# Kernel optimization log

Hardware: AMD Instinct MI355X
Metric: run time of the kernel (lower is better)

Reference implementation:

```python
import jax, jax.numpy as jnp
import numpy as np

B, S, D, H, P, K = 2, 1025, 1024, 16, 1024, 32
HD = D // H
G = int(np.sqrt(P))
TEMP = 0.1
CANTOR_W = 0.3
SCALE = HD ** -0.5
EPS_LN = 1e-5


def _layernorm(x, w, b):
    m = jnp.mean(x, axis=-1, keepdims=True)
    v = jnp.mean((x - m) ** 2, axis=-1, keepdims=True)
    return (x - m) * jax.lax.rsqrt(v + EPS_LN) * w + b


def _l2norm(x):
    n = jnp.sqrt(jnp.sum(x * x, axis=-1, keepdims=True))
    return x / jnp.maximum(n, 1e-12)


def _cantor_bias():
    idx = np.arange(P)
    xg, yg = idx % G, idx // G
    s = xg + yg
    z = (s * (s + 1) // 2 + yg).astype(np.float32)
    fp = z / max(z.max(), 1.0)
    dist = np.abs(fp[None, :] - fp[:, None])
    aff = 1.0 - dist
    np.fill_diagonal(aff, -1e9)
    return jnp.asarray(aff * CANTOR_W, dtype=jnp.float32)


def setup_inputs() -> dict:
    key = jax.random.key(0)
    ks = jax.random.split(key, 16)
    std = 0.02
    def w(k, *shape):
        return jax.random.normal(k, shape, dtype=jnp.float32) * std
    inp = {
        'x': jax.random.normal(ks[0], (B, S, D), dtype=jnp.float32),
        'norm1_w': jnp.ones((D,), jnp.float32), 'norm1_b': jnp.zeros((D,), jnp.float32),
        'rq_w': w(ks[1], D, D), 'rq_b': jnp.zeros((D,), jnp.float32),
        'rk_w': w(ks[2], D, D), 'rk_b': jnp.zeros((D,), jnp.float32),
        'pos_bias': _cantor_bias(),
        'qkv_w': w(ks[3], 3 * D, D), 'qkv_b': jnp.zeros((3 * D,), jnp.float32),
        'proj_w': w(ks[4], D, D), 'proj_b': jnp.zeros((D,), jnp.float32),
        'norm2_w': jnp.ones((D,), jnp.float32), 'norm2_b': jnp.zeros((D,), jnp.float32),
        'fc1_w': w(ks[5], 4 * D, D), 'fc1_b': jnp.zeros((4 * D,), jnp.float32),
        'fc2_w': w(ks[6], D, 4 * D), 'fc2_b': jnp.zeros((D,), jnp.float32),
    }
    return inp


def reference(x, norm1_w, norm1_b, rq_w, rq_b, rk_w, rk_b, pos_bias,
              qkv_w, qkv_b, proj_w, proj_b, norm2_w, norm2_b,
              fc1_w, fc1_b, fc2_w, fc2_b):
    x_norm = _layernorm(x, norm1_w, norm1_b)
    # ---- router: content-based top-k wormhole routes over patches ----
    xp = x_norm[:, 1:, :]                                   # [B,P,D]
    q_r = _l2norm(xp @ rq_w.T + rq_b)
    k_r = _l2norm(xp @ rk_w.T + rk_b)
    scores = jnp.einsum('bpd,bqd->bpq', q_r, k_r) + pos_bias[None]
    eye = jnp.eye(P, dtype=bool)
    scores = jnp.where(eye[None], -1e9, scores)
    topk_scores, routes = jax.lax.top_k(scores / TEMP, K)   # [B,P,K]
    route_w = jax.nn.softmax(topk_scores, axis=-1)          # [B,P,K]
    # ---- qkv ----
    qkv = (x_norm @ qkv_w.T + qkv_b).reshape(B, S, 3, H, HD)
    qkv = jnp.transpose(qkv, (2, 0, 3, 1, 4))               # [3,B,H,S,hd]
    Q, Kf, V = qkv[0], qkv[1], qkv[2]
    # CLS token: dense attention over all positions
    Qc = Q[:, :, :1, :]
    attn_cls = jax.nn.softmax(jnp.einsum('bhqd,bhkd->bhqk', Qc, Kf) * SCALE, axis=-1)
    out_cls = jnp.einsum('bhqk,bhkd->bhqd', attn_cls, V)    # [B,H,1,hd]
    # Patches: sparse gather attention via wormhole routes
    Qp, Kp, Vp = Q[:, :, 1:], Kf[:, :, 1:], V[:, :, 1:]     # [B,H,P,hd]
    gather = jax.vmap(lambda t, r: t[:, r])                 # t:[H,P,hd], r:[P,K] -> [H,P,K,hd]
    Kg = gather(Kp, routes)                                  # [B,H,P,K,hd]
    Vg = gather(Vp, routes)
    sp = jnp.einsum('bhpd,bhpkd->bhpk', Qp, Kg) * SCALE
    sp = sp + jnp.clip(jnp.log(route_w), -10.0, None)[:, None]
    attn_p = jax.nn.softmax(sp, axis=-1)
    out_p = jnp.einsum('bhpk,bhpkd->bhpd', attn_p, Vg)      # [B,H,P,hd]
    out = jnp.concatenate([out_cls, out_p], axis=2)          # [B,H,S,hd]
    out = jnp.transpose(out, (0, 2, 1, 3)).reshape(B, S, D)
    x = x + (out @ proj_w.T + proj_b)
    h = _layernorm(x, norm2_w, norm2_b)
    h = jax.nn.gelu(h @ fc1_w.T + fc1_b, approximate=False)
    x = x + (h @ fc2_w.T + fc2_b)
    return x
```

## Files before the change

### kernel.cpp

```cpp
#include <hip/hip_runtime.h>
#include <hip/hip_bf16.h>
#include <math.h>

typedef unsigned short u16;
typedef __attribute__((ext_vector_type(8))) short short8;
typedef __attribute__((ext_vector_type(4))) float f32x4;

#define B_ 2
#define S_ 1025
#define D_ 1024
#define H_ 16
#define HD_ 64
#define P_ 1024
#define K_ 32
#define NS_ 16

static constexpr float TEMP_ = 0.1f;
static constexpr float SCALE_ = 0.125f;
static constexpr float EPS_LN_ = 1e-5f;

__device__ __forceinline__ float bf2f(u16 u) {
  unsigned int t = ((unsigned int)u) << 16;
  float f;
  __builtin_memcpy(&f, &t, 4);
  return f;
}
__device__ __forceinline__ u16 f2bf(float f) {
  __hip_bfloat16 h = __float2bfloat16(f);
  u16 u;
  __builtin_memcpy(&u, &h, 2);
  return u;
}
__device__ __forceinline__ float gelu_f(float x) {
  return 0.5f * x * (1.0f + erff(x * 0.70710678118654752f));
}

typedef __attribute__((address_space(1))) const unsigned int gas_u32;
typedef __attribute__((address_space(3))) unsigned int las_u32;
__device__ __forceinline__ void g2l16(const void* g, void* l) {
  __builtin_amdgcn_global_load_lds((gas_u32*)g, (las_u32*)l, 16, 0, 0);
}

__global__ __launch_bounds__(256) void conv4_kernel(
    const float* __restrict__ s0, int n0, const float* __restrict__ s1, int n1,
    const float* __restrict__ s2, int n2, const float* __restrict__ s3, int n3,
    u16* __restrict__ dst) {
  const int e = (blockIdx.x * 256 + threadIdx.x) * 4;
  const float* src;
  int off;
  if (e < n0) { src = s0; off = e; }
  else if (e < n0 + n1) { src = s1; off = e - n0; }
  else if (e < n0 + n1 + n2) { src = s2; off = e - n0 - n1; }
  else if (e < n0 + n1 + n2 + n3) { src = s3; off = e - n0 - n1 - n2; }
  else return;
  float4 t = *reinterpret_cast<const float4*>(src + off);
  ushort4 o;
  o.x = f2bf(t.x); o.y = f2bf(t.y); o.z = f2bf(t.z); o.w = f2bf(t.w);
  *reinterpret_cast<ushort4*>(dst + e) = o;
}

__global__ __launch_bounds__(256) void init_addb(const float* __restrict__ a,
                                                 const float* __restrict__ bias,
                                                 float* __restrict__ out) {
  const long long base = (long long)blockIdx.x * D_;
#pragma unroll
  for (int u = 0; u < 4; ++u) {
    int d = threadIdx.x + u * 256;
    out[base + d] = a[base + d] + bias[d];
  }
}

__global__ __launch_bounds__(256) void init_scores(const float* __restrict__ pos,
                                                   float* __restrict__ scores) {
  const int bp = blockIdx.x;
  const int p = bp & (P_ - 1);
  const long long base = (long long)bp * P_;
#pragma unroll
  for (int u = 0; u < 4; ++u) {
    int q = threadIdx.x + u * 256;
    float v = pos[(long long)p * P_ + q];
    if (p == q) v = -1e9f;
    scores[base + q] = v;
  }
}

__device__ __forceinline__ float block_sum256(float v, float* red4) {
  for (int off = 32; off > 0; off >>= 1) v += __shfl_down(v, off);
  if ((threadIdx.x & 63) == 0) red4[threadIdx.x >> 6] = v;
  __syncthreads();
  float r = red4[0] + red4[1] + red4[2] + red4[3];
  __syncthreads();
  return r;
}
__device__ __forceinline__ float block_max256(float v, float* red4) {
  for (int off = 32; off > 0; off >>= 1) v = fmaxf(v, __shfl_down(v, off));
  if ((threadIdx.x & 63) == 0) red4[threadIdx.x >> 6] = v;
  __syncthreads();
  float r = fmaxf(fmaxf(red4[0], red4[1]), fmaxf(red4[2], red4[3]));
  __syncthreads();
  return r;
}

__global__ __launch_bounds__(256) void ln_kernel(const float* __restrict__ x,
                                                 const float* __restrict__ w,
                                                 const float* __restrict__ b,
                                                 u16* __restrict__ out) {
  __shared__ float red4[4];
  const long long base = (long long)blockIdx.x * D_;
  float v[4];
  float s = 0.f, ss = 0.f;
#pragma unroll
  for (int u = 0; u < 4; ++u) {
    int d = threadIdx.x + u * 256;
    float f = x[base + d];
    v[u] = f; s += f; ss += f * f;
  }
  float tot = block_sum256(s, red4);
  float tot2 = block_sum256(ss, red4);
  float mean = tot * (1.0f / D_);
  float var = tot2 * (1.0f / D_) - mean * mean;
  float rstd = rsqrtf(var + EPS_LN_);
#pragma unroll
  for (int u = 0; u < 4; ++u) {
    int d = threadIdx.x + u * 256;
    out[base + d] = f2bf((v[u] - mean) * rstd * w[d] + b[d]);
  }
}

__global__ __launch_bounds__(256) void l2norm2_kernel(u16* __restrict__ qr,
                                                      u16* __restrict__ kr) {
  __shared__ float red4[4];
  const int row = blockIdx.x;
  u16* x = (row < 2048) ? qr + (long long)row * D_
                        : kr + (long long)(row - 2048) * D_;
  float v[4];
  float ss = 0.f;
#pragma unroll
  for (int u = 0; u < 4; ++u) {
    int d = threadIdx.x + u * 256;
    v[u] = bf2f(x[d]);
    ss += v[u] * v[u];
  }
  float tot = block_sum256(ss, red4);
  float inv = 1.0f / fmaxf(sqrtf(tot), 1e-12f);
#pragma unroll
  for (int u = 0; u < 4; ++u) {
    int d = threadIdx.x + u * 256;
    x[d] = f2bf(v[u] * inv);
  }
}

template <int MODE>
__device__ __forceinline__ void gemm_body(
    u16* sA, u16* sW,
    const u16* __restrict__ A, long long a_off, const u16* __restrict__ W,
    int N, int M, int Kd, int klen, int rpb, long long a_bs, long long w_bs,
    const float* __restrict__ bias, const float* __restrict__ bias2, int bias_off,
    u16* __restrict__ outU, u16* __restrict__ outU2, float* __restrict__ outF,
    int bx, int by, int bz) {
  const int tid = threadIdx.x;
  const int lane = tid & 63;
  const int q4 = lane >> 4;
  const int r16 = lane & 15;
  const int wave = tid >> 6;
  const int wr = (wave >> 1) * 64;
  const int wc = (wave & 1) * 64;
  const int row0 = by * 128;
  const int col0 = bx * 128;
  const int batch = row0 / rpb;
  const u16* Ab = A + a_off + (long long)batch * a_bs +
                  (long long)(row0 - batch * rpb) * Kd;
  const u16* Wb = W + (long long)batch * w_bs + (long long)col0 * Kd;
  const int rmax = N - 1 - row0;
  const int srow = tid >> 3;
  const int kx = ((tid & 7) ^ (srow & 7)) * 8;
  const int kbeg = bz * klen;
  const int niter = klen >> 6;
  f32x4 acc[4][4] = {};
  for (int it = 0; it < niter; ++it) {
    const int k0 = kbeg + it * 64;
#pragma unroll
    for (int c = 0; c < 4; ++c) {
      const int rg = c * 32 + srow;
      g2l16(Ab + (long long)min(rg, rmax) * Kd + kx + k0, &sA[c * 2048 + tid * 8]);
      g2l16(Wb + (long long)rg * Kd + kx + k0, &sW[c * 2048 + tid * 8]);
    }
    __builtin_amdgcn_s_waitcnt(0);
    __syncthreads();
#pragma unroll
    for (int s = 0; s < 2; ++s) {
      short8 a[4], b[4];
      const int ks = ((s * 4 + q4) ^ (r16 & 7)) * 8;
#pragma unroll
      for (int i = 0; i < 4; ++i) {
        a[i] = *reinterpret_cast<const short8*>(&sA[(wr + i * 16 + r16) * 64 + ks]);
        b[i] = *reinterpret_cast<const short8*>(&sW[(wc + i * 16 + r16) * 64 + ks]);
      }
#pragma unroll
      for (int i = 0; i < 4; ++i)
#pragma unroll
        for (int j = 0; j < 4; ++j)
          acc[i][j] = __builtin_amdgcn_mfma_f32_16x16x32_bf16(a[i], b[j],
                                                              acc[i][j], 0, 0, 0);
    }
    __syncthreads();
  }
#pragma unroll
  for (int i = 0; i < 4; ++i) {
#pragma unroll
    for (int reg = 0; reg < 4; ++reg) {
      const int n = row0 + wr + i * 16 + q4 * 4 + reg;
      if (n >= N) continue;
      const long long nrow = (long long)n * M;
#pragma unroll
      for (int j = 0; j < 4; ++j) {
        const int m = col0 + wc + j * 16 + r16;
        float v = acc[i][j][reg];
        if (MODE == 0) {
          if (m < 1024) outU[(long long)n * 1024 + m] = f2bf(v + bias[m]);
          else outU2[(long long)n * 1024 + m - 1024] = f2bf(v + bias2[m - 1024]);
        } else if (MODE == 2) {
          outU[nrow + m] = f2bf(v + bias[bias_off + m]);
        } else if (MODE == 3) {
          outU[nrow + m] = f2bf(gelu_f(v + bias[bias_off + m]));
        } else {
          unsafeAtomicAdd(&outF[nrow + m], v);
        }
      }
    }
  }
}

template <int MODE>
__global__ __launch_bounds__(256, 4) void mfma_gemm(
    const u16* __restrict__ A, long long a_off, const u16* __restrict__ W,
    int N, int M, int Kd, int klen, int rpb, long long a_bs, long long w_bs,
    const float* __restrict__ bias, const float* __restrict__ bias2, int bias_off,
    u16* __restrict__ outU, u16* __restrict__ outU2, float* __restrict__ outF) {
  __shared__ u16 sA[128 * 64];
  __shared__ u16 sW[128 * 64];
  gemm_body<MODE>(sA, sW, A, a_off, W, N, M, Kd, klen, rpb, a_bs, w_bs,
                  bias, bias2, bias_off, outU, outU2, outF,
                  blockIdx.x, blockIdx.y, blockIdx.z);
}

__global__ __launch_bounds__(256, 4) void fused_rqk_qkv(
    const u16* __restrict__ xnorm, const u16* __restrict__ wslot,
    const float* __restrict__ rq_b, const float* __restrict__ rk_b,
    const float* __restrict__ qkv_b,
    u16* __restrict__ qr, u16* __restrict__ kr, u16* __restrict__ qkvb) {
  __shared__ u16 sA[128 * 64];
  __shared__ u16 sW[128 * 64];
  const int id = blockIdx.x;
  if (id < 256) {
    gemm_body<0>(sA, sW, xnorm, 1024LL, wslot,
                 2048, 2048, 1024, 1024, 1024, (long long)S_ * D_, 0LL,
                 rq_b, rk_b, 0, qr, kr, nullptr, id & 15, id >> 4, 0);
  } else {
    const int id2 = id - 256;
    gemm_body<2>(sA, sW, xnorm, 0LL, wslot + (2 << 20),
                 2050, 3072, 1024, 1024, 2050, 0LL, 0LL,
                 qkv_b, nullptr, 0, qkvb, nullptr, nullptr, id2 % 24, id2 / 24, 0);
  }
}

__global__ __launch_bounds__(256) void topk_kernel(const float* __restrict__ scores,
                                                   int* __restrict__ routes,
                                                   float* __restrict__ logw) {
  const int row = blockIdx.x * 4 + (threadIdx.x >> 6);
  const int lane = threadIdx.x & 63;
  const float* sr = scores + (long long)row * P_;
  float v[16];
#pragma unroll
  for (int j = 0; j < 16; ++j) v[j] = sr[j * 64 + lane];
  float selv = 0.f;
  int seli = 0;
  for (int t = 0; t < K_; ++t) {
    float bv = v[0];
    int bj = 0;
#pragma unroll
    for (int j = 1; j < 16; ++j)
      if (v[j] > bv) { bv = v[j]; bj = j; }
    int bi = bj * 64 + lane;
#pragma unroll
    for (int off = 1; off < 64; off <<= 1) {
      float ov = __shfl_xor(bv, off);
      int oi = __shfl_xor(bi, off);
      if (ov > bv || (ov == bv && oi < bi)) { bv = ov; bi = oi; }
    }
    if (lane == t) { selv = bv; seli = bi; }
    if ((bi & 63) == lane) v[bi >> 6] = -3.0e38f;
  }
  const float sc = selv * (1.0f / TEMP_);
  const float mt = __shfl(sc, 0);
  float e = (lane < K_) ? expf(sc - mt) : 0.f;
  float sum = e;
#pragma unroll
  for (int off = 1; off < 64; off <<= 1) sum += __shfl_xor(sum, off);
  if (lane < K_) {
    const float lw = sc - mt - logf(sum);
    logw[(long long)row * K_ + lane] = fmaxf(lw, -10.0f);
    routes[(long long)row * K_ + lane] = seli;
  }
}

__global__ __launch_bounds__(256) void attn_cls_p1(const u16* __restrict__ qkv,
                                                   float* __restrict__ part) {
  __shared__ float qs[HD_];
  __shared__ float lg[65];
  __shared__ float red4[4];
  __shared__ float sacc[4][HD_];
  const int ck = blockIdx.x;
  const int bh = blockIdx.y;
  const int b = bh >> 4, h = bh & 15;
  const int tid = threadIdx.x;
  const int lane = tid & 63;
  const int wv = tid >> 6;
  const int s0 = ck * 65;
  const int rows = min(65, S_ - s0);
  const long long base = (long long)b * S_ * 3072;
  if (tid < HD_) qs[tid] = bf2f(qkv[base + h * HD_ + tid]);
  __syncthreads();
  float lmax = -3.0e38f;
  if (tid < rows) {
    const u16* kp = qkv + base + (long long)(s0 + tid) * 3072 + 1024 + h * HD_;
    float d = 0.f;
#pragma unroll
    for (int c = 0; c < 8; ++c) {
      short8 kv = *reinterpret_cast<const short8*>(kp + c * 8);
#pragma unroll
      for (int e = 0; e < 8; ++e) d += qs[c * 8 + e] * bf2f((u16)kv[e]);
    }
    d *= SCALE_;
    lg[tid] = d;
    lmax = d;
  }
  const float m = block_max256(lmax, red4);
  float e = 0.f;
  if (tid < rows) {
    e = expf(lg[tid] - m);
    lg[tid] = e;
  }
  const float l = block_sum256(e, red4);
  __syncthreads();
  float acc = 0.f;
  for (int r = wv; r < rows; r += 4)
    acc += lg[r] * bf2f(qkv[base + (long long)(s0 + r) * 3072 + 2048 + h * HD_ + lane]);
  sacc[wv][lane] = acc;
  __syncthreads();
  float* pc = part + ((long long)bh * NS_ + ck) * 66;
  if (tid < HD_)
    pc[tid] = sacc[0][tid] + sacc[1][tid] + sacc[2][tid] + sacc[3][tid];
  if (tid == 64) pc[64] = m;
  if (tid == 65) pc[65] = l;
}

__global__ __launch_bounds__(64) void attn_cls_p2(const float* __restrict__ part,
                                                  u16* __restrict__ out) {
  const int bh = blockIdx.x;
  const int b = bh >> 4, h = bh & 15;
  const int tid = threadIdx.x;
  const float* pb = part + (long long)bh * NS_ * 66;
  float M = -3.0e38f;
#pragma unroll
  for (int c = 0; c < NS_; ++c) M = fmaxf(M, pb[c * 66 + 64]);
  float L = 0.f, a = 0.f;
#pragma unroll
  for (int c = 0; c < NS_; ++c) {
    const float w = expf(pb[c * 66 + 64] - M);
    L += pb[c * 66 + 65] * w;
    a += pb[c * 66 + tid] * w;
  }
  out[(long long)b * S_ * D_ + h * HD_ + tid] = f2bf(a / L);
}

__global__ __launch_bounds__(64) void attn_patch_kernel(const u16* __restrict__ qkv,
                                                        const int* __restrict__ routes,
                                                        const float* __restrict__ logw,
                                                        u16* __restrict__ out) {
  __shared__ float qs[HD_];
  __shared__ float wk[K_];
  __shared__ int sidx[K_];
  const int bid = blockIdx.x;
  const int h = bid & 15;
  const int p = (bid >> 4) & (P_ - 1);
  const int b = bid >> 14;
  const int tid = threadIdx.x;
  const long long base = (long long)b * S_ * 3072;
  qs[tid] = bf2f(qkv[base + (long long)(1 + p) * 3072 + h * HD_ + tid]);
  __syncthreads();
  float lg = -3.0e38f;
  if (tid < K_) {
    const long long ro = ((long long)(b * P_ + p)) * K_ + tid;
    const int r = routes[ro];
    sidx[tid] = r;
    const u16* kp = qkv + base + (long long)(1 + r) * 3072 + 1024 + h * HD_;
    float d = 0.f;
#pragma unroll
    for (int c = 0; c < 8; ++c) {
      short8 kv = *reinterpret_cast<const short8*>(kp + c * 8);
#pragma unroll
      for (int e = 0; e < 8; ++e) d += qs[c * 8 + e] * bf2f((u16)kv[e]);
    }
    lg = d * SCALE_ + logw[ro];
  }
  float m = lg;
#pragma unroll
  for (int off = 1; off < 32; off <<= 1) m = fmaxf(m, __shfl_xor(m, off));
  float e = (tid < K_) ? expf(lg - m) : 0.f;
  float sum = e;
#pragma unroll
  for (int off = 1; off < 32; off <<= 1) sum += __shfl_xor(sum, off);
  if (tid < K_) wk[tid] = e / sum;
  __syncthreads();
  float acc = 0.f;
#pragma unroll 4
  for (int k = 0; k < K_; ++k)
    acc += wk[k] * bf2f(qkv[base + (long long)(1 + sidx[k]) * 3072 + 2048 + h * HD_ + tid]);
  out[((long long)b * S_ + 1 + p) * D_ + h * HD_ + tid] = f2bf(acc);
}

extern "C" void kernel_launch(void* const* d_in, const int* in_sizes, int n_in,
                              void* d_out, int out_size, void* d_ws, size_t ws_size,
                              hipStream_t stream) {
  const float* x      = (const float*)d_in[0];
  const float* n1w    = (const float*)d_in[1];
  const float* n1b    = (const float*)d_in[2];
  const float* rq_w   = (const float*)d_in[3];
  const float* rq_b   = (const float*)d_in[4];
  const float* rk_w   = (const float*)d_in[5];
  const float* rk_b   = (const float*)d_in[6];
  const float* pos    = (const float*)d_in[7];
  const float* qkv_w  = (const float*)d_in[8];
  const float* qkv_b  = (const float*)d_in[9];
  const float* proj_w = (const float*)d_in[10];
  const float* proj_b = (const float*)d_in[11];
  const float* n2w    = (const float*)d_in[12];
  const float* n2b    = (const float*)d_in[13];
  const float* fc1_w  = (const float*)d_in[14];
  const float* fc1_b  = (const float*)d_in[15];
  const float* fc2_w  = (const float*)d_in[16];
  const float* fc2_b  = (const float*)d_in[17];
  float* out = (float*)d_out;

  char* mem = (char*)d_ws;
  int*   routes = (int*)mem;
  float* logw   = (float*)(mem + 262144);
  float* part   = (float*)(mem + 524288);
  u16*   wslot  = (u16*)(mem + 786432);
  u16*   xnorm  = (u16*)(mem + 17563648);
  u16*   qr     = (u16*)(mem + 21762048);
  u16*   attn   = qr;
  u16*   qkvb   = (u16*)(mem + 25960448);
  u16*   kr     = (u16*)(mem + 38555648);
  u16*   hbuf   = qkvb;
  float* scores = (float*)(mem + 42758144);
  float* x1     = (float*)(mem + 42758144);

  ln_kernel<<<B_ * S_, 256, 0, stream>>>(x, n1w, n1b, xnorm);

  conv4_kernel<<<6144, 256, 0, stream>>>(rq_w, 1 << 20, rk_w, 1 << 20,
                                         qkv_w, 3 << 20, proj_w, 1 << 20, wslot);

  fused_rqk_qkv<<<664, 256, 0, stream>>>(xnorm, wslot, rq_b, rk_b, qkv_b,
                                         qr, kr, qkvb);

  l2norm2_kernel<<<4096, 256, 0, stream>>>(qr, kr);

  init_scores<<<B_ * P_, 256, 0, stream>>>(pos, scores);
  mfma_gemm<5><<<dim3(8, 16, 2), 256, 0, stream>>>(qr, 0LL, kr,
      2048, 1024, 1024, 512, 1024, 1LL << 20, 1LL << 20,
      nullptr, nullptr, 0, nullptr, nullptr, scores);

  topk_kernel<<<512, 256, 0, stream>>>(scores, routes, logw);

  attn_cls_p1<<<dim3(NS_, B_ * H_), 256, 0, stream>>>(qkvb, part);
  attn_cls_p2<<<B_ * H_, 64, 0, stream>>>(part, attn);
  attn_patch_kernel<<<B_ * P_ * H_, 64, 0, stream>>>(qkvb, routes, logw, attn);

  init_addb<<<B_ * S_, 256, 0, stream>>>(x, proj_b, x1);
  mfma_gemm<5><<<dim3(8, 17, 2), 256, 0, stream>>>(attn, 0LL, wslot + (5 << 20),
      2050, 1024, 1024, 512, 2050, 0LL, 0LL,
      nullptr, nullptr, 0, nullptr, nullptr, x1);

  conv4_kernel<<<8192, 256, 0, stream>>>(fc1_w, 1 << 22, fc2_w, 1 << 22,
                                         nullptr, 0, nullptr, 0, wslot);

  ln_kernel<<<B_ * S_, 256, 0, stream>>>(x1, n2w, n2b, xnorm);

  mfma_gemm<3><<<dim3(32, 17), 256, 0, stream>>>(xnorm, 0LL, wslot,
      2050, 4096, 1024, 1024, 2050, 0LL, 0LL,
      fc1_b, nullptr, 0, hbuf, nullptr, nullptr);
  init_addb<<<B_ * S_, 256, 0, stream>>>(x1, fc2_b, out);
  mfma_gemm<5><<<dim3(8, 17, 4), 256, 0, stream>>>(hbuf, 0LL, wslot + (1 << 22),
      2050, 1024, 4096, 1024, 2050, 0LL, 0LL,
      nullptr, nullptr, 0, nullptr, nullptr, out);
}
```

Baseline: 399.9 us.

## Double-buffer GEMM LDS tiles to overlap global loads with MFMA compute

Converts the shared GEMM main loop into a two-stage LDS ping-pong. The next K-tile is issued with async global-to-LDS loads before the current tile is computed, using partial vmcnt waits and raw barriers instead of full syncthreads. This is meant to hide global memory latency behind the MFMA work. LDS use per block doubles to 64 KB, so the launch bounds drop from 4 to 2 blocks per CU, which reduces occupancy.

After: 433.6 us. +8.4%, slower.

```diff
diff --git a/kernel.cpp b/kernel.cpp
--- a/kernel.cpp
+++ b/kernel.cpp
@@ -177,24 +177,43 @@
   const int kbeg = bz * klen;
   const int niter = klen >> 6;
   f32x4 acc[4][4] = {};
-  for (int it = 0; it < niter; ++it) {
-    const int k0 = kbeg + it * 64;
+  {
+    const int k0 = kbeg;
 #pragma unroll
     for (int c = 0; c < 4; ++c) {
       const int rg = c * 32 + srow;
       g2l16(Ab + (long long)min(rg, rmax) * Kd + kx + k0, &sA[c * 2048 + tid * 8]);
       g2l16(Wb + (long long)rg * Kd + kx + k0, &sW[c * 2048 + tid * 8]);
     }
-    __builtin_amdgcn_s_waitcnt(0);
-    __syncthreads();
+  }
+  int cur = 0;
+  for (int it = 0; it < niter; ++it) {
+    if (it + 1 < niter) {
+      const int k0 = kbeg + (it + 1) * 64;
+      const int nb = (cur ^ 1) * 8192;
+#pragma unroll
+      for (int c = 0; c < 4; ++c) {
+        const int rg = c * 32 + srow;
+        g2l16(Ab + (long long)min(rg, rmax) * Kd + kx + k0,
+              &sA[nb + c * 2048 + tid * 8]);
+        g2l16(Wb + (long long)rg * Kd + kx + k0, &sW[nb + c * 2048 + tid * 8]);
+      }
+      asm volatile("s_waitcnt vmcnt(8)" ::: "memory");
+    } else {
+      asm volatile("s_waitcnt vmcnt(0)" ::: "memory");
+    }
+    __builtin_amdgcn_s_barrier();
+    const int cb = cur * 8192;
 #pragma unroll
     for (int s = 0; s < 2; ++s) {
       short8 a[4], b[4];
       const int ks = ((s * 4 + q4) ^ (r16 & 7)) * 8;
 #pragma unroll
       for (int i = 0; i < 4; ++i) {
-        a[i] = *reinterpret_cast<const short8*>(&sA[(wr + i * 16 + r16) * 64 + ks]);
-        b[i] = *reinterpret_cast<const short8*>(&sW[(wc + i * 16 + r16) * 64 + ks]);
+        a[i] = *reinterpret_cast<const short8*>(
+            &sA[cb + (wr + i * 16 + r16) * 64 + ks]);
+        b[i] = *reinterpret_cast<const short8*>(
+            &sW[cb + (wc + i * 16 + r16) * 64 + ks]);
       }
 #pragma unroll
       for (int i = 0; i < 4; ++i)
@@ -203,7 +222,9 @@
           acc[i][j] = __builtin_amdgcn_mfma_f32_16x16x32_bf16(a[i], b[j],
                                                               acc[i][j], 0, 0, 0);
     }
-    __syncthreads();
+    asm volatile("s_waitcnt lgkmcnt(0)" ::: "memory");
+    __builtin_amdgcn_s_barrier();
+    cur ^= 1;
   }
 #pragma unroll
   for (int i = 0; i < 4; ++i) {
@@ -232,25 +253,25 @@
 }
 
 template <int MODE>
-__global__ __launch_bounds__(256, 4) void mfma_gemm(
+__global__ __launch_bounds__(256, 2) void mfma_gemm(
     const u16* __restrict__ A, long long a_off, const u16* __restrict__ W,
     int N, int M, int Kd, int klen, int rpb, long long a_bs, long long w_bs,
     const float* __restrict__ bias, const float* __restrict__ bias2, int bias_off,
     u16* __restrict__ outU, u16* __restrict__ outU2, float* __restrict__ outF) {
-  __shared__ u16 sA[128 * 64];
-  __shared__ u16 sW[128 * 64];
+  __shared__ u16 sA[2 * 128 * 64];
+  __shared__ u16 sW[2 * 128 * 64];
   gemm_body<MODE>(sA, sW, A, a_off, W, N, M, Kd, klen, rpb, a_bs, w_bs,
                   bias, bias2, bias_off, outU, outU2, outF,
                   blockIdx.x, blockIdx.y, blockIdx.z);
 }
 
-__global__ __launch_bounds__(256, 4) void fused_rqk_qkv(
+__global__ __launch_bounds__(256, 2) void fused_rqk_qkv(
     const u16* __restrict__ xnorm, const u16* __restrict__ wslot,
     const float* __restrict__ rq_b, const float* __restrict__ rk_b,
     const float* __restrict__ qkv_b,
     u16* __restrict__ qr, u16* __restrict__ kr, u16* __restrict__ qkvb) {
-  __shared__ u16 sA[128 * 64];
-  __shared__ u16 sW[128 * 64];
+  __shared__ u16 sA[2 * 128 * 64];
+  __shared__ u16 sW[2 * 128 * 64];
   const int id = blockIdx.x;
   if (id < 256) {
     gemm_body<0>(sA, sW, xnorm, 1024LL, wslot,
```
